# Performance work log

Hardware: AMD Instinct MI355X
Metric: run time of the kernel (lower is better)

Reference implementation:

```python
import jax, jax.numpy as jnp
import numpy as np

N = 4
SEGMENTS = 16
IN_F = 256
OUT_F = 256
BATCH = 512


def chebyshev_lobatto(n):
    # Chebyshev-Lobatto interpolation nodes on [-1, 1]
    k = jnp.arange(n, dtype=jnp.float32)
    return -jnp.cos(jnp.pi * k / (n - 1))


def lagrange_basis(x, nodes):
    # x: [B, In]; returns basis values [B, In, n]
    n = nodes.shape[0]
    cols = []
    for j in range(n):  # n is a small static constant (4)
        terms = [(x - nodes[m]) / (nodes[j] - nodes[m]) for m in range(n) if m != j]
        cols.append(jnp.prod(jnp.stack(terms, axis=0), axis=0))
    return jnp.stack(cols, axis=-1)


def setup_inputs() -> dict:
    key = jax.random.key(0)
    k1, k2 = jax.random.split(key)
    x = jax.random.uniform(k1, (BATCH, IN_F), dtype=jnp.float32, minval=-1.0, maxval=1.0)
    w = jax.random.uniform(
        k2, (OUT_F, IN_F, (N - 1) * SEGMENTS + 1), dtype=jnp.float32, minval=-1.0, maxval=1.0
    )
    return {"x": x, "w": w, "n": N, "segments": SEGMENTS}


def reference(x, w, n, segments):
    nodes = chebyshev_lobatto(n)
    # segment id per element, clamped to [0, segments-1]
    id_min = jnp.clip(((x + 1.0) / 2.0 * segments).astype(jnp.int32), 0, segments - 1)
    id_max = id_min + 1
    wid_min = id_min * (n - 1)  # start of weight slice; slice length == n
    # segment boundaries in x-space: eta(i) = i/segments * 2 - 1
    x_min = id_min.astype(x.dtype) / segments * 2.0 - 1.0
    x_max = id_max.astype(x.dtype) / segments * 2.0 - 1.0
    # rescale x into [-1, 1] within its segment
    x_in = 2.0 * (x - x_min) / (x_max - x_min) - 1.0
    basis = lagrange_basis(x_in, nodes)  # [B, In, n]
    # gather per-element weight slice: w_g[b,i,j,o] = w[o, i, wid_min[b,i]+j]
    idx = wid_min[..., None] + jnp.arange(n)  # [B, In, n]
    w_t = jnp.transpose(w, (1, 2, 0))  # [In, K, Out]
    in_f = w.shape[1]
    w_g = w_t[jnp.arange(in_f)[None, :, None], idx]  # [B, In, n, Out]
    # interpolate and sum over in_features (matches einsum 'ijk,jkli->jl')
    return jnp.einsum("bin,bino->bo", basis, w_g)
```

## Files before the change

### kernel.cpp

```cpp
#include <hip/hip_runtime.h>


typedef _Float16 h2 __attribute__((ext_vector_type(2)));

#define INF     256
#define OUTF    256
#define WSTRIDE 49
#define OSTRIDE (INF * WSTRIDE)
#define PSLICE  (512 * 256)

__global__ __launch_bounds__(512, 2)
void pp_partial(const float* __restrict__ x, const float* __restrict__ w,
                float* __restrict__ part) {
    __shared__ unsigned int wt[8192];

    const int tid  = threadIdx.x;
    const int wave = tid >> 6, lane = tid & 63;
    const int isplit = blockIdx.x & 15;
    const int otile  = blockIdx.x >> 4;
    const int i_base = isplit * 16;
    const int o_base = otile * 16;
    const int b      = wave * 64 + lane;

    const float4* xp = (const float4*)(x + (size_t)b * INF + i_base);
    float4 xv0 = xp[0], xv1 = xp[1], xv2 = xp[2], xv3 = xp[3];

    _Float16* wth = (_Float16*)wt;
    for (int r = wave; r < 256; r += 8) {
        const int i_loc = r >> 4, o_loc = r & 15;
        const int op = o_loc >> 1, e = o_loc & 1;
        float v = 0.0f;
        if (lane < 49)
            v = w[(size_t)(o_base + o_loc) * OSTRIDE
                  + (size_t)(i_base + i_loc) * WSTRIDE + lane];
        const _Float16 hv = (_Float16)v;
        const int s1 = lane / 3, j1 = lane - 3 * s1;
        const int hb = (i_loc * 8 + op) * 16;
        if (lane < 49) {
            if (s1 < 16)            wth[(hb + s1) * 8 + e * 4 + j1] = hv;
            if (j1 == 0 && lane)    wth[(hb + s1 - 1) * 8 + e * 4 + 3] = hv;
        }
    }

    float xs[16] = {xv0.x, xv0.y, xv0.z, xv0.w, xv1.x, xv1.y, xv1.z, xv1.w,
                    xv2.x, xv2.y, xv2.z, xv2.w, xv3.x, xv3.y, xv3.z, xv3.w};
    int sseg[16]; h2 cA[16], cB[16];
    #pragma unroll
    for (int i = 0; i < 16; ++i) {
        float xx = xs[i];
        int id = (int)((xx + 1.0f) * 8.0f);
        id = id < 0 ? 0 : (id > 15 ? 15 : id);
        float u = (xx - ((float)id * 0.125f - 1.0f)) * 16.0f - 1.0f;
        float a = u + 1.0f, b2 = u + 0.5f, cc = u - 0.5f, d = u - 1.0f;
        float c0 = b2 * cc * d  * (-2.0f / 3.0f);
        float c1 = a  * cc * d  * ( 4.0f / 3.0f);
        float c2 = a  * b2 * d  * (-4.0f / 3.0f);
        float c3 = a  * b2 * cc * ( 2.0f / 3.0f);
        h2 pA; pA[0] = (_Float16)c0; pA[1] = (_Float16)c1;
        h2 pB; pB[0] = (_Float16)c2; pB[1] = (_Float16)c3;
        cA[i] = pA; cB[i] = pB; sseg[i] = id;
    }

    __syncthreads();

    float acc[16];
    #pragma unroll
    for (int q = 0; q < 16; ++q) acc[q] = 0.0f;

    #pragma unroll
    for (int i = 0; i < 16; ++i) {
        const unsigned int* p = &wt[(i * 128 + sseg[i]) * 4];
        #pragma unroll
        for (int op = 0; op < 8; ++op) {
            uint4 v = *(const uint4*)(p + op * 64);
            acc[2*op]   = __builtin_amdgcn_fdot2(__builtin_bit_cast(h2, v.x), cA[i],
                                                 acc[2*op],   false);
            acc[2*op]   = __builtin_amdgcn_fdot2(__builtin_bit_cast(h2, v.y), cB[i],
                                                 acc[2*op],   false);
            acc[2*op+1] = __builtin_amdgcn_fdot2(__builtin_bit_cast(h2, v.z), cA[i],
                                                 acc[2*op+1], false);
            acc[2*op+1] = __builtin_amdgcn_fdot2(__builtin_bit_cast(h2, v.w), cB[i],
                                                 acc[2*op+1], false);
        }
    }

    float4* pp = (float4*)(part + (size_t)isplit * PSLICE
                                + (size_t)b * 256 + o_base);
    pp[0] = make_float4(acc[0],  acc[1],  acc[2],  acc[3]);
    pp[1] = make_float4(acc[4],  acc[5],  acc[6],  acc[7]);
    pp[2] = make_float4(acc[8],  acc[9],  acc[10], acc[11]);
    pp[3] = make_float4(acc[12], acc[13], acc[14], acc[15]);
}

__global__ __launch_bounds__(256)
void pp_reduce(const float* __restrict__ part, float* __restrict__ out) {
    const size_t off4 = (size_t)blockIdx.x * 256 + threadIdx.x;
    const float4* p4 = (const float4*)part;
    float4 s = make_float4(0.f, 0.f, 0.f, 0.f);
    #pragma unroll
    for (int k = 0; k < 16; ++k) {
        float4 v = p4[(size_t)k * (PSLICE / 4) + off4];
        s.x += v.x; s.y += v.y; s.z += v.z; s.w += v.w;
    }
    ((float4*)out)[off4] = s;
}

extern "C" void kernel_launch(void* const* d_in, const int* in_sizes, int n_in,
                              void* d_out, int out_size, void* d_ws, size_t ws_size,
                              hipStream_t stream) {
    const float* x = (const float*)d_in[0];
    const float* w = (const float*)d_in[1];
    float* out  = (float*)d_out;
    float* part = (float*)d_ws;
    (void)ws_size; (void)n_in; (void)in_sizes; (void)out_size;

    pp_partial<<<dim3(256), 512, 0, stream>>>(x, w, part);
    pp_reduce<<<dim3(128), 256, 0, stream>>>(part, out);
}
```

Measured before the change: 87.72 us.

## Split into prep, main, and reduce kernels with pre-packed fp16 weights

Adds a prep kernel that converts weights to a packed fp16 per-segment layout and precomputes per-element basis coefficients and segment ids into workspace. The main kernel then loads weight tiles into LDS with global_load_lds and has each lane handle one output over a loop of batch rows, with a 32-way input split. The reduce kernel sums 32 partial slices instead of 16. This removes the scattered fp32 weight loads and in-kernel conversion, at the cost of an extra launch, extra workspace traffic, and a larger reduction.

```diff
diff --git a/kernel.cpp b/kernel.cpp
--- a/kernel.cpp
+++ b/kernel.cpp
@@ -8,88 +8,99 @@
 #define WSTRIDE 49
 #define OSTRIDE (INF * WSTRIDE)
 #define PSLICE  (512 * 256)
+#define WE_U2   (256 * 16 * 256)
+#define BT_U4   (512 * 256)
 
-__global__ __launch_bounds__(512, 2)
-void pp_partial(const float* __restrict__ x, const float* __restrict__ w,
-                float* __restrict__ part) {
-    __shared__ unsigned int wt[8192];
+#define GLOAD16(gptr, lptr)                                                         \
+  __builtin_amdgcn_global_load_lds(                                                 \
+      (const __attribute__((address_space(1))) unsigned int*)(gptr),                \
+      (__attribute__((address_space(3))) unsigned int*)(lptr), 16, 0, 0)
+
+__global__ __launch_bounds__(256)
+void pp_prep(const float* __restrict__ x, const float* __restrict__ w,
+             uint2* __restrict__ we, uint4* __restrict__ bt) {
+    const int blk = blockIdx.x;
+    if (blk < 256) {
+        const int i = blk, o = threadIdx.x;
+        const float* src = w + (size_t)o * OSTRIDE + i * WSTRIDE;
+        float t[49];
+        #pragma unroll
+        for (int k = 0; k < 49; ++k) t[k] = src[k];
+        #pragma unroll
+        for (int s = 0; s < 16; ++s) {
+            auto p0 = __builtin_amdgcn_cvt_pkrtz(t[3*s],   t[3*s+1]);
+            auto p1 = __builtin_amdgcn_cvt_pkrtz(t[3*s+2], t[3*s+3]);
+            uint2 v;
+            v.x = __builtin_bit_cast(unsigned int, p0);
+            v.y = __builtin_bit_cast(unsigned int, p1);
+            we[((size_t)i * 16 + s) * 256 + o] = v;
+        }
+    } else {
+        const int e = (blk - 256) * 1024 + threadIdx.x * 4;
+        float4 xv = *(const float4*)(x + e);
+        const float xs[4] = {xv.x, xv.y, xv.z, xv.w};
+        #pragma unroll
+        for (int q = 0; q < 4; ++q) {
+            float xx = xs[q];
+            int id = (int)((xx + 1.0f) * 8.0f);
+            id = id < 0 ? 0 : (id > 15 ? 15 : id);
+            float u = (xx - ((float)id * 0.125f - 1.0f)) * 16.0f - 1.0f;
+            float a = u + 1.0f, b2 = u + 0.5f, cc = u - 0.5f, d = u - 1.0f;
+            float c0 = b2 * cc * d  * (-2.0f / 3.0f);
+            float c1 = a  * cc * d  * ( 4.0f / 3.0f);
+            float c2 = a  * b2 * d  * (-4.0f / 3.0f);
+            float c3 = a  * b2 * cc * ( 2.0f / 3.0f);
+            auto pA = __builtin_amdgcn_cvt_pkrtz(c0, c1);
+            auto pB = __builtin_amdgcn_cvt_pkrtz(c2, c3);
+            uint4 v;
+            v.x = __builtin_bit_cast(unsigned int, pA);
+            v.y = __builtin_bit_cast(unsigned int, pB);
+            v.z = (unsigned int)id;
+            v.w = 0u;
+            bt[e + q] = v;
+        }
+    }
+}
+
+__global__ __launch_bounds__(256, 2)
+void pp_main(const uint2* __restrict__ we, const uint4* __restrict__ bt,
+             float* __restrict__ part) {
+    __shared__ uint2 wt[8192];
 
     const int tid  = threadIdx.x;
-    const int wave = tid >> 6, lane = tid & 63;
-    const int isplit = blockIdx.x & 15;
-    const int otile  = blockIdx.x >> 4;
-    const int i_base = isplit * 16;
-    const int o_base = otile * 16;
-    const int b      = wave * 64 + lane;
+    const int wave = __builtin_amdgcn_readfirstlane(tid >> 6);
+    const int lane = tid & 63;
+    const int i_base = blockIdx.x * 8;
+    const int o_base = blockIdx.y * 64;
+    const int b0     = blockIdx.z * 128 + wave * 32;
 
-    const float4* xp = (const float4*)(x + (size_t)b * INF + i_base);
-    float4 xv0 = xp[0], xv1 = xp[1], xv2 = xp[2], xv3 = xp[3];
-
-    _Float16* wth = (_Float16*)wt;
-    for (int r = wave; r < 256; r += 8) {
-        const int i_loc = r >> 4, o_loc = r & 15;
-        const int op = o_loc >> 1, e = o_loc & 1;
-        float v = 0.0f;
-        if (lane < 49)
-            v = w[(size_t)(o_base + o_loc) * OSTRIDE
-                  + (size_t)(i_base + i_loc) * WSTRIDE + lane];
-        const _Float16 hv = (_Float16)v;
-        const int s1 = lane / 3, j1 = lane - 3 * s1;
-        const int hb = (i_loc * 8 + op) * 16;
-        if (lane < 49) {
-            if (s1 < 16)            wth[(hb + s1) * 8 + e * 4 + j1] = hv;
-            if (j1 == 0 && lane)    wth[(hb + s1 - 1) * 8 + e * 4 + 3] = hv;
-        }
+    #pragma unroll
+    for (int it = 0; it < 16; ++it) {
+        const int u = it * 256 + tid;
+        const int i = u >> 9, s = (u >> 5) & 15, g = u & 31;
+        const unsigned int* gp = (const unsigned int*)we
+            + ((((size_t)(i_base + i) * 16 + s) * 256) + o_base + g * 2) * 2;
+        GLOAD16(gp, (unsigned int*)wt + (size_t)u * 4);
     }
-
-    float xs[16] = {xv0.x, xv0.y, xv0.z, xv0.w, xv1.x, xv1.y, xv1.z, xv1.w,
-                    xv2.x, xv2.y, xv2.z, xv2.w, xv3.x, xv3.y, xv3.z, xv3.w};
-    int sseg[16]; h2 cA[16], cB[16];
-    #pragma unroll
-    for (int i = 0; i < 16; ++i) {
-        float xx = xs[i];
-        int id = (int)((xx + 1.0f) * 8.0f);
-        id = id < 0 ? 0 : (id > 15 ? 15 : id);
-        float u = (xx - ((float)id * 0.125f - 1.0f)) * 16.0f - 1.0f;
-        float a = u + 1.0f, b2 = u + 0.5f, cc = u - 0.5f, d = u - 1.0f;
-        float c0 = b2 * cc * d  * (-2.0f / 3.0f);
-        float c1 = a  * cc * d  * ( 4.0f / 3.0f);
-        float c2 = a  * b2 * d  * (-4.0f / 3.0f);
-        float c3 = a  * b2 * cc * ( 2.0f / 3.0f);
-        h2 pA; pA[0] = (_Float16)c0; pA[1] = (_Float16)c1;
-        h2 pB; pB[0] = (_Float16)c2; pB[1] = (_Float16)c3;
-        cA[i] = pA; cB[i] = pB; sseg[i] = id;
-    }
-
     __syncthreads();
 
-    float acc[16];
-    #pragma unroll
-    for (int q = 0; q < 16; ++q) acc[q] = 0.0f;
+    const uint4* btp = bt + ((size_t)b0 * 256 + i_base);
+    float* pout = part + (size_t)blockIdx.x * PSLICE + o_base + lane;
 
-    #pragma unroll
-    for (int i = 0; i < 16; ++i) {
-        const unsigned int* p = &wt[(i * 128 + sseg[i]) * 4];
+    for (int bb = 0; bb < 32; ++bb) {
+        const uint4* be = btp + (size_t)bb * 256;
+        float acc = 0.0f;
         #pragma unroll
-        for (int op = 0; op < 8; ++op) {
-            uint4 v = *(const uint4*)(p + op * 64);
-            acc[2*op]   = __builtin_amdgcn_fdot2(__builtin_bit_cast(h2, v.x), cA[i],
-                                                 acc[2*op],   false);
-            acc[2*op]   = __builtin_amdgcn_fdot2(__builtin_bit_cast(h2, v.y), cB[i],
-                                                 acc[2*op],   false);
-            acc[2*op+1] = __builtin_amdgcn_fdot2(__builtin_bit_cast(h2, v.z), cA[i],
-                                                 acc[2*op+1], false);
-            acc[2*op+1] = __builtin_amdgcn_fdot2(__builtin_bit_cast(h2, v.w), cB[i],
-                                                 acc[2*op+1], false);
+        for (int i = 0; i < 8; ++i) {
+            const uint4 B = be[i];
+            const h2 cA = __builtin_bit_cast(h2, B.x);
+            const h2 cB = __builtin_bit_cast(h2, B.y);
+            const uint2 wv = wt[((i * 16 + (int)B.z) << 6) + lane];
+            acc = __builtin_amdgcn_fdot2(__builtin_bit_cast(h2, wv.x), cA, acc, false);
+            acc = __builtin_amdgcn_fdot2(__builtin_bit_cast(h2, wv.y), cB, acc, false);
         }
+        pout[(size_t)(b0 + bb) * 256] = acc;
     }
-
-    float4* pp = (float4*)(part + (size_t)isplit * PSLICE
-                                + (size_t)b * 256 + o_base);
-    pp[0] = make_float4(acc[0],  acc[1],  acc[2],  acc[3]);
-    pp[1] = make_float4(acc[4],  acc[5],  acc[6],  acc[7]);
-    pp[2] = make_float4(acc[8],  acc[9],  acc[10], acc[11]);
-    pp[3] = make_float4(acc[12], acc[13], acc[14], acc[15]);
 }
 
 __global__ __launch_bounds__(256)
@@ -98,7 +109,7 @@
     const float4* p4 = (const float4*)part;
     float4 s = make_float4(0.f, 0.f, 0.f, 0.f);
     #pragma unroll
-    for (int k = 0; k < 16; ++k) {
+    for (int k = 0; k < 32; ++k) {
         float4 v = p4[(size_t)k * (PSLICE / 4) + off4];
         s.x += v.x; s.y += v.y; s.z += v.z; s.w += v.w;
     }
@@ -110,10 +121,14 @@
                               hipStream_t stream) {
     const float* x = (const float*)d_in[0];
     const float* w = (const float*)d_in[1];
-    float* out  = (float*)d_out;
-    float* part = (float*)d_ws;
+    float* out = (float*)d_out;
+    uint2* we  = (uint2*)d_ws;
+    uint4* bt  = (uint4*)((char*)d_ws + (size_t)WE_U2 * 8);
+    float* part = (float*)((char*)d_ws + (size_t)WE_U2 * 8
+                                       + (size_t)BT_U4 * 16);
     (void)ws_size; (void)n_in; (void)in_sizes; (void)out_size;
 
-    pp_partial<<<dim3(256), 512, 0, stream>>>(x, w, part);
+    pp_prep<<<dim3(384), 256, 0, stream>>>(x, w, we, bt);
+    pp_main<<<dim3(32, 4, 4), 256, 0, stream>>>(we, bt, part);
     pp_reduce<<<dim3(128), 256, 0, stream>>>(part, out);
 }
```

Result: slower. 93.82 us (+7.0%).
